# Kernel tuning notes

Measured on AMD Instinct MI355X. Metric: run time of the kernel, lower is better.

The kernel has to match this reference:

```python
import jax, jax.numpy as jnp
import numpy as np

N_NODES = 100000
N_EDGES = 1600000
D_IN = 64
D_OUT = 64


def setup_inputs() -> dict:
    key = jax.random.key(0)
    k1, k2, k3, k4 = jax.random.split(key, 4)
    x = jax.random.normal(k1, (N_NODES, D_IN), dtype=jnp.float32)
    edge_index = jax.random.randint(k2, (2, N_EDGES), 0, N_NODES, dtype=jnp.int64)
    W = jax.random.normal(k3, (D_OUT, D_IN), dtype=jnp.float32) * (1.0 / np.sqrt(D_IN))
    b = jax.random.normal(k4, (D_OUT,), dtype=jnp.float32) * 0.01
    return {"x": x, "edge_index": edge_index, "W": W, "b": b}


def reference(x, edge_index, W, b):
    num_nodes = x.shape[0]
    row, col = edge_index[0], edge_index[1]
    # degree of each node as a destination (scatter_add of ones over row)
    deg = jax.ops.segment_sum(jnp.ones(row.shape[0], dtype=x.dtype), row,
                              num_segments=num_nodes)
    # deg^-0.5 with inf (deg==0) replaced by 0
    deg_inv_sqrt = jnp.where(deg > 0, jax.lax.rsqrt(jnp.maximum(deg, 1.0)) * jnp.where(deg > 0, 1.0, 0.0), 0.0)
    deg_inv_sqrt = jnp.where(deg > 0, deg ** -0.5, 0.0)
    # gather source features, scale by source norm, scatter-add to destinations
    weighted = x[col] * deg_inv_sqrt[col][:, None]          # [E, D_IN]
    agg = jax.ops.segment_sum(weighted, row, num_segments=num_nodes)  # [N, D_IN]
    agg = agg * deg_inv_sqrt[:, None]
    # linear + relu (torch Linear: y = agg @ W.T + b)
    return jax.nn.relu(agg @ W.T + b)
```

## Files before the change

kernel.cpp:

```cpp
#include <hip/hip_runtime.h>

#define N_NODES 100000
#define N_EDGES 1600000
#define D 64

#define FSHIFT 5
#define FNODES 32
#define NFB 3125
#define CAPF 768

#define CSHIFT 11
#define CNODES 2048
#define NCB 49
#define CCAP 36864
#define FPC 64

#define CHUNK 4096
#define EPT 16
#define NCHUNKA 391
#define NCHUNKB 9
#define NSB (NCB * NCHUNKB)
#define NXF 1563

#define COLBITS 17
#define COLMASK 0x1FFFF

#define CCUR_OFF   0
#define FCUR_OFF   256
#define INIT_BYTES 12756
#define DINV_OFF   16384
#define Y_OFF      417792
#define CPAIRS_OFF 13217792
#define FPAIRS_OFF 20443136

typedef float fvec4 __attribute__((ext_vector_type(4)));

__device__ __forceinline__ unsigned f2bf(float f) {
    unsigned bits = __float_as_uint(f);
    return (bits + 0x7FFFu + ((bits >> 16) & 1u)) >> 16;
}

__global__ __launch_bounds__(256) void scatA_kernel(const int* __restrict__ row,
                                                    const int* __restrict__ col,
                                                    int* __restrict__ ccur,
                                                    int* __restrict__ cpairs) {
    __shared__ int lcnt[NCB];
    int t = threadIdx.x;
    int base = blockIdx.x * CHUNK;
    if (t < NCB) lcnt[t] = 0;
    __syncthreads();
    int r[EPT], c[EPT], pos[EPT];
#pragma unroll
    for (int i = 0; i < EPT; ++i) {
        int e = base + i * 256 + t;
        if (e < N_EDGES) {
            r[i] = row[e];
            c[i] = col[e];
            pos[i] = atomicAdd(&lcnt[r[i] >> CSHIFT], 1);
        } else r[i] = -1;
    }
    __syncthreads();
    if (t < NCB) {
        int cc = lcnt[t];
        if (cc) lcnt[t] = t * CCAP + atomicAdd(&ccur[t], cc);
    }
    __syncthreads();
#pragma unroll
    for (int i = 0; i < EPT; ++i) {
        if (r[i] >= 0) {
            int cb = r[i] >> CSHIFT;
            int rl = r[i] & (CNODES - 1);
            cpairs[lcnt[cb] + pos[i]] = (rl << COLBITS) | c[i];
        }
    }
}

__global__ __launch_bounds__(1024) void dinv_kernel(const int* __restrict__ cpairs,
                                                    const int* __restrict__ ccur,
                                                    float* __restrict__ dinv) {
    __shared__ int hist[CNODES];
    int t = threadIdx.x;
    int cb = blockIdx.x;
    for (int i = t; i < CNODES; i += 1024) hist[i] = 0;
    __syncthreads();
    int beg = cb * CCAP;
    int end = beg + ccur[cb];
    for (int k = beg + t; k < end; k += 1024)
        atomicAdd(&hist[cpairs[k] >> COLBITS], 1);
    __syncthreads();
    for (int i = t; i < CNODES; i += 1024) {
        int n = (cb << CSHIFT) + i;
        if (n < N_NODES) {
            int d = hist[i];
            dinv[n] = (d > 0) ? rsqrtf((float)d) : 0.0f;
        }
    }
}

__global__ __launch_bounds__(256) void sbxf_kernel(
        const int* __restrict__ cpairs, const int* __restrict__ ccur,
        int* __restrict__ fcur, int* __restrict__ fpairs,
        const float* __restrict__ x, const float* __restrict__ W,
        const float* __restrict__ dinv, unsigned short* __restrict__ y) {
    __shared__ __align__(16) float smem[2 * 64 * 68 + 64];
    int t = threadIdx.x;
    int blk = blockIdx.x;
    if (blk < NSB) {
        int* lcnt = (int*)smem;
        int cb = blk / NCHUNKB;
        int k  = blk % NCHUNKB;
        int beg = cb * CCAP + k * CHUNK;
        int end = cb * CCAP + ccur[cb];
        if (end > beg + CHUNK) end = beg + CHUNK;
        if (t < FPC) lcnt[t] = 0;
        __syncthreads();
        int pc[EPT], pos[EPT];
#pragma unroll
        for (int i = 0; i < EPT; ++i) {
            int e = beg + i * 256 + t;
            if (e < end) {
                pc[i] = cpairs[e];
                pos[i] = atomicAdd(&lcnt[pc[i] >> (COLBITS + FSHIFT)], 1);
            } else pc[i] = -1;
        }
        __syncthreads();
        if (t < FPC) {
            int cc = lcnt[t];
            if (cc) {
                int fb = (cb << 6) + t;
                lcnt[t] = fb * CAPF + atomicAdd(&fcur[fb], cc);
            }
        }
        __syncthreads();
#pragma unroll
        for (int i = 0; i < EPT; ++i) {
            if (pc[i] >= 0) {
                int fl = pc[i] >> (COLBITS + FSHIFT);
                int rl5 = (pc[i] >> COLBITS) & (FNODES - 1);
                fpairs[lcnt[fl] + pos[i]] = (rl5 << COLBITS) | (pc[i] & COLMASK);
            }
        }
        return;
    }
    float* XT = smem;
    float* WT = smem + 64 * 68;
    float* dl = smem + 2 * 64 * 68;
    int b = blk - NSB;
    int nb0 = b << 6;
    for (int i = t; i < D * D; i += 256) {
        int j = i >> 6, d = i & 63;
        WT[d * 68 + j] = W[i];
    }
    if (t < 64) {
        int g = nb0 + t;
        dl[t] = (g < N_NODES) ? dinv[g] : 0.0f;
    }
    for (int i = t; i < 64 * D; i += 256) {
        int n = i >> 6, d = i & 63;
        int g = nb0 + n;
        XT[d * 68 + n] = (g < N_NODES) ? x[(size_t)g * D + d] : 0.0f;
    }
    __syncthreads();
    int tj = t & 15, tn = t >> 4;
    float4 a0 = {0,0,0,0}, a1 = {0,0,0,0}, a2 = {0,0,0,0}, a3 = {0,0,0,0};
#pragma unroll 8
    for (int d = 0; d < D; ++d) {
        float4 xv = *(const float4*)&XT[d * 68 + tn * 4];
        float4 wv = *(const float4*)&WT[d * 68 + tj * 4];
        a0.x = fmaf(xv.x, wv.x, a0.x); a0.y = fmaf(xv.x, wv.y, a0.y);
        a0.z = fmaf(xv.x, wv.z, a0.z); a0.w = fmaf(xv.x, wv.w, a0.w);
        a1.x = fmaf(xv.y, wv.x, a1.x); a1.y = fmaf(xv.y, wv.y, a1.y);
        a1.z = fmaf(xv.y, wv.z, a1.z); a1.w = fmaf(xv.y, wv.w, a1.w);
        a2.x = fmaf(xv.z, wv.x, a2.x); a2.y = fmaf(xv.z, wv.y, a2.y);
        a2.z = fmaf(xv.z, wv.z, a2.z); a2.w = fmaf(xv.z, wv.w, a2.w);
        a3.x = fmaf(xv.w, wv.x, a3.x); a3.y = fmaf(xv.w, wv.y, a3.y);
        a3.z = fmaf(xv.w, wv.z, a3.z); a3.w = fmaf(xv.w, wv.w, a3.w);
    }
    int jb = tj * 4;
#pragma unroll
    for (int s = 0; s < 4; ++s) {
        int g = nb0 + tn * 4 + s;
        if (g < N_NODES) {
            float scv = dl[tn * 4 + s];
            float4 a = (s == 0) ? a0 : (s == 1) ? a1 : (s == 2) ? a2 : a3;
            unsigned lo = f2bf(a.x * scv) | (f2bf(a.y * scv) << 16);
            unsigned hi = f2bf(a.z * scv) | (f2bf(a.w * scv) << 16);
            *(uint2*)(y + (size_t)g * D + jb) = make_uint2(lo, hi);
        }
    }
}

__global__ __launch_bounds__(256) void mega_kernel(
        const int* __restrict__ fpairs, const int* __restrict__ fcur,
        const unsigned short* __restrict__ y,
        const float* __restrict__ bias, float* __restrict__ out) {
    __shared__ int hist[FNODES];
    __shared__ int sc[FNODES];
    __shared__ int lrptr[FNODES + 1];
    __shared__ int lcur[FNODES];
    __shared__ float dl[FNODES];
    __shared__ int lds_scol[CAPF];
    int t = threadIdx.x;
    int b = blockIdx.x;
    int beg = b * CAPF;
    int cnt = fcur[b];
    if (t < FNODES) hist[t] = 0;
    __syncthreads();
    for (int k = t; k < cnt; k += 256)
        atomicAdd(&hist[fpairs[beg + k] >> COLBITS], 1);
    __syncthreads();
    if (t < FNODES) sc[t] = hist[t];
    __syncthreads();
    for (int off = 1; off < FNODES; off <<= 1) {
        int v = (t < FNODES && t >= off) ? sc[t - off] : 0;
        __syncthreads();
        if (t < FNODES) sc[t] += v;
        __syncthreads();
    }
    if (t < FNODES) {
        lrptr[t + 1] = sc[t];
        lcur[t] = sc[t] - hist[t];
        dl[t] = (hist[t] > 0) ? rsqrtf((float)hist[t]) : 0.0f;
    }
    if (t == 0) lrptr[0] = 0;
    __syncthreads();
    for (int k = t; k < cnt; k += 256) {
        int p = fpairs[beg + k];
        int pos = atomicAdd(&lcur[p >> COLBITS], 1);
        lds_scol[pos] = p & COLMASK;
    }
    __syncthreads();
    int wave = t >> 6;
    int lane = t & 63;
    int g = lane >> 3;
    int q = lane & 7;
    float bj[8];
    {
        float4 b0 = *(const float4*)(bias + q * 8);
        float4 b1 = *(const float4*)(bias + q * 8 + 4);
        bj[0] = b0.x; bj[1] = b0.y; bj[2] = b0.z; bj[3] = b0.w;
        bj[4] = b1.x; bj[5] = b1.y; bj[6] = b1.z; bj[7] = b1.w;
    }
    for (int ln = wave; ln < FNODES; ln += 4) {
        int s = lrptr[ln], e2 = lrptr[ln + 1];
        float a[8];
#pragma unroll
        for (int i = 0; i < 8; ++i) a[i] = 0.0f;
        for (int k = s; k < e2; k += 32) {
#pragma unroll
            for (int u = 0; u < 4; ++u) {
                int e = k + u * 8 + g;
                if (e < e2) {
                    int c = lds_scol[e];
                    uint4 v = *(const uint4*)(y + (size_t)c * D + q * 8);
                    a[0] += __uint_as_float(v.x << 16);
                    a[1] += __uint_as_float(v.x & 0xffff0000u);
                    a[2] += __uint_as_float(v.y << 16);
                    a[3] += __uint_as_float(v.y & 0xffff0000u);
                    a[4] += __uint_as_float(v.z << 16);
                    a[5] += __uint_as_float(v.z & 0xffff0000u);
                    a[6] += __uint_as_float(v.w << 16);
                    a[7] += __uint_as_float(v.w & 0xffff0000u);
                }
            }
        }
#pragma unroll
        for (int m = 8; m <= 32; m <<= 1) {
#pragma unroll
            for (int i = 0; i < 8; ++i)
                a[i] += __shfl_xor(a[i], m);
        }
        float dv = dl[ln];
        int n = (b << FSHIFT) + ln;
        if (g < 2) {
            int o = g * 4;
            fvec4 r;
            r.x = fmaxf(fmaf(dv, a[o + 0], bj[o + 0]), 0.0f);
            r.y = fmaxf(fmaf(dv, a[o + 1], bj[o + 1]), 0.0f);
            r.z = fmaxf(fmaf(dv, a[o + 2], bj[o + 2]), 0.0f);
            r.w = fmaxf(fmaf(dv, a[o + 3], bj[o + 3]), 0.0f);
            __builtin_nontemporal_store(r, (fvec4*)(out + (size_t)n * D + q * 8 + o));
        }
    }
}

extern "C" void kernel_launch(void* const* d_in, const int* in_sizes, int n_in,
                              void* d_out, int out_size, void* d_ws, size_t ws_size,
                              hipStream_t stream) {
    const float* x    = (const float*)d_in[0];
    const int*   eidx = (const int*)d_in[1];
    const float* W    = (const float*)d_in[2];
    const float* b    = (const float*)d_in[3];
    float* out = (float*)d_out;
    char* ws = (char*)d_ws;

    const int* row = eidx;
    const int* col = eidx + N_EDGES;

    int*   ccur   = (int*)  (ws + CCUR_OFF);
    int*   fcur   = (int*)  (ws + FCUR_OFF);
    float* dinv   = (float*)(ws + DINV_OFF);
    unsigned short* y = (unsigned short*)(ws + Y_OFF);
    int*   cpairs = (int*)  (ws + CPAIRS_OFF);
    int*   fpairs = (int*)  (ws + FPAIRS_OFF);

    hipMemsetAsync(ws, 0, INIT_BYTES, stream);
    scatA_kernel<<<NCHUNKA, 256, 0, stream>>>(row, col, ccur, cpairs);
    dinv_kernel<<<NCB, 1024, 0, stream>>>(cpairs, ccur, dinv);
    sbxf_kernel<<<NSB + NXF, 256, 0, stream>>>(cpairs, ccur, fcur, fpairs, x, W, dinv, y);
    mega_kernel<<<NFB, 256, 0, stream>>>(fpairs, fcur, y, b, out);
}
```

Baseline: 186.3 us.

## Merge dinv into second pass, split xform across passes, apply source norm in gather

The dense transform no longer depends on degree normalisation; instead each edge's source dinv is loaded in the final aggregation kernel and applied via fma. This lets the transform tiles be split between the first scatter kernel and the second kernel, and the dinv histogram is folded into the second kernel, cutting one launch. The cost is an extra random dinv gather per edge and extra LDS in the aggregation kernel. The mega kernel also assumes at most 768 pairs per bucket, which is the existing CAPF capacity.

```diff
diff --git a/kernel.cpp b/kernel.cpp
--- a/kernel.cpp
+++ b/kernel.cpp
@@ -21,6 +21,8 @@
 #define NCHUNKB 9
 #define NSB (NCB * NCHUNKB)
 #define NXF 1563
+#define XFA 700
+#define XFB (NXF - XFA)
 
 #define COLBITS 17
 #define COLMASK 0x1FFFF
@@ -40,120 +42,14 @@
     return (bits + 0x7FFFu + ((bits >> 16) & 1u)) >> 16;
 }
 
-__global__ __launch_bounds__(256) void scatA_kernel(const int* __restrict__ row,
-                                                    const int* __restrict__ col,
-                                                    int* __restrict__ ccur,
-                                                    int* __restrict__ cpairs) {
-    __shared__ int lcnt[NCB];
-    int t = threadIdx.x;
-    int base = blockIdx.x * CHUNK;
-    if (t < NCB) lcnt[t] = 0;
-    __syncthreads();
-    int r[EPT], c[EPT], pos[EPT];
-#pragma unroll
-    for (int i = 0; i < EPT; ++i) {
-        int e = base + i * 256 + t;
-        if (e < N_EDGES) {
-            r[i] = row[e];
-            c[i] = col[e];
-            pos[i] = atomicAdd(&lcnt[r[i] >> CSHIFT], 1);
-        } else r[i] = -1;
-    }
-    __syncthreads();
-    if (t < NCB) {
-        int cc = lcnt[t];
-        if (cc) lcnt[t] = t * CCAP + atomicAdd(&ccur[t], cc);
-    }
-    __syncthreads();
-#pragma unroll
-    for (int i = 0; i < EPT; ++i) {
-        if (r[i] >= 0) {
-            int cb = r[i] >> CSHIFT;
-            int rl = r[i] & (CNODES - 1);
-            cpairs[lcnt[cb] + pos[i]] = (rl << COLBITS) | c[i];
-        }
-    }
-}
-
-__global__ __launch_bounds__(1024) void dinv_kernel(const int* __restrict__ cpairs,
-                                                    const int* __restrict__ ccur,
-                                                    float* __restrict__ dinv) {
-    __shared__ int hist[CNODES];
-    int t = threadIdx.x;
-    int cb = blockIdx.x;
-    for (int i = t; i < CNODES; i += 1024) hist[i] = 0;
-    __syncthreads();
-    int beg = cb * CCAP;
-    int end = beg + ccur[cb];
-    for (int k = beg + t; k < end; k += 1024)
-        atomicAdd(&hist[cpairs[k] >> COLBITS], 1);
-    __syncthreads();
-    for (int i = t; i < CNODES; i += 1024) {
-        int n = (cb << CSHIFT) + i;
-        if (n < N_NODES) {
-            int d = hist[i];
-            dinv[n] = (d > 0) ? rsqrtf((float)d) : 0.0f;
-        }
-    }
-}
-
-__global__ __launch_bounds__(256) void sbxf_kernel(
-        const int* __restrict__ cpairs, const int* __restrict__ ccur,
-        int* __restrict__ fcur, int* __restrict__ fpairs,
+__device__ __forceinline__ void xform_tile(int nb0, float* smem, int t,
         const float* __restrict__ x, const float* __restrict__ W,
-        const float* __restrict__ dinv, unsigned short* __restrict__ y) {
-    __shared__ __align__(16) float smem[2 * 64 * 68 + 64];
-    int t = threadIdx.x;
-    int blk = blockIdx.x;
-    if (blk < NSB) {
-        int* lcnt = (int*)smem;
-        int cb = blk / NCHUNKB;
-        int k  = blk % NCHUNKB;
-        int beg = cb * CCAP + k * CHUNK;
-        int end = cb * CCAP + ccur[cb];
-        if (end > beg + CHUNK) end = beg + CHUNK;
-        if (t < FPC) lcnt[t] = 0;
-        __syncthreads();
-        int pc[EPT], pos[EPT];
-#pragma unroll
-        for (int i = 0; i < EPT; ++i) {
-            int e = beg + i * 256 + t;
-            if (e < end) {
-                pc[i] = cpairs[e];
-                pos[i] = atomicAdd(&lcnt[pc[i] >> (COLBITS + FSHIFT)], 1);
-            } else pc[i] = -1;
-        }
-        __syncthreads();
-        if (t < FPC) {
-            int cc = lcnt[t];
-            if (cc) {
-                int fb = (cb << 6) + t;
-                lcnt[t] = fb * CAPF + atomicAdd(&fcur[fb], cc);
-            }
-        }
-        __syncthreads();
-#pragma unroll
-        for (int i = 0; i < EPT; ++i) {
-            if (pc[i] >= 0) {
-                int fl = pc[i] >> (COLBITS + FSHIFT);
-                int rl5 = (pc[i] >> COLBITS) & (FNODES - 1);
-                fpairs[lcnt[fl] + pos[i]] = (rl5 << COLBITS) | (pc[i] & COLMASK);
-            }
-        }
-        return;
-    }
+        unsigned short* __restrict__ y) {
     float* XT = smem;
     float* WT = smem + 64 * 68;
-    float* dl = smem + 2 * 64 * 68;
-    int b = blk - NSB;
-    int nb0 = b << 6;
     for (int i = t; i < D * D; i += 256) {
         int j = i >> 6, d = i & 63;
         WT[d * 68 + j] = W[i];
-    }
-    if (t < 64) {
-        int g = nb0 + t;
-        dl[t] = (g < N_NODES) ? dinv[g] : 0.0f;
     }
     for (int i = t; i < 64 * D; i += 256) {
         int n = i >> 6, d = i & 63;
@@ -181,18 +77,128 @@
     for (int s = 0; s < 4; ++s) {
         int g = nb0 + tn * 4 + s;
         if (g < N_NODES) {
-            float scv = dl[tn * 4 + s];
             float4 a = (s == 0) ? a0 : (s == 1) ? a1 : (s == 2) ? a2 : a3;
-            unsigned lo = f2bf(a.x * scv) | (f2bf(a.y * scv) << 16);
-            unsigned hi = f2bf(a.z * scv) | (f2bf(a.w * scv) << 16);
+            unsigned lo = f2bf(a.x) | (f2bf(a.y) << 16);
+            unsigned hi = f2bf(a.z) | (f2bf(a.w) << 16);
             *(uint2*)(y + (size_t)g * D + jb) = make_uint2(lo, hi);
+        }
+    }
+}
+
+__global__ __launch_bounds__(256) void saxf_kernel(
+        const int* __restrict__ row, const int* __restrict__ col,
+        int* __restrict__ ccur, int* __restrict__ cpairs,
+        const float* __restrict__ x, const float* __restrict__ W,
+        unsigned short* __restrict__ y) {
+    __shared__ __align__(16) float smem[2 * 64 * 68];
+    int t = threadIdx.x;
+    int blk = blockIdx.x;
+    if (blk >= NCHUNKA) {
+        xform_tile((blk - NCHUNKA) << 6, smem, t, x, W, y);
+        return;
+    }
+    int* lcnt = (int*)smem;
+    int base = blk * CHUNK;
+    if (t < NCB) lcnt[t] = 0;
+    __syncthreads();
+    int r[EPT], c[EPT], pos[EPT];
+#pragma unroll
+    for (int i = 0; i < EPT; ++i) {
+        int e = base + i * 256 + t;
+        if (e < N_EDGES) {
+            r[i] = row[e];
+            c[i] = col[e];
+            pos[i] = atomicAdd(&lcnt[r[i] >> CSHIFT], 1);
+        } else r[i] = -1;
+    }
+    __syncthreads();
+    if (t < NCB) {
+        int cc = lcnt[t];
+        if (cc) lcnt[t] = t * CCAP + atomicAdd(&ccur[t], cc);
+    }
+    __syncthreads();
+#pragma unroll
+    for (int i = 0; i < EPT; ++i) {
+        if (r[i] >= 0) {
+            int cb = r[i] >> CSHIFT;
+            int rl = r[i] & (CNODES - 1);
+            cpairs[lcnt[cb] + pos[i]] = (rl << COLBITS) | c[i];
+        }
+    }
+}
+
+__global__ __launch_bounds__(256) void dsbxf_kernel(
+        const int* __restrict__ cpairs, const int* __restrict__ ccur,
+        int* __restrict__ fcur, int* __restrict__ fpairs,
+        float* __restrict__ dinv,
+        const float* __restrict__ x, const float* __restrict__ W,
+        unsigned short* __restrict__ y) {
+    __shared__ __align__(16) float smem[2 * 64 * 68];
+    int t = threadIdx.x;
+    int blk = blockIdx.x;
+    if (blk < NCB) {
+        int* hist = (int*)smem;
+        int cb = blk;
+        for (int i = t; i < CNODES; i += 256) hist[i] = 0;
+        __syncthreads();
+        int beg = cb * CCAP;
+        int end = beg + ccur[cb];
+        for (int k = beg + t; k < end; k += 256)
+            atomicAdd(&hist[cpairs[k] >> COLBITS], 1);
+        __syncthreads();
+        for (int i = t; i < CNODES; i += 256) {
+            int n = (cb << CSHIFT) + i;
+            if (n < N_NODES) {
+                int d = hist[i];
+                dinv[n] = (d > 0) ? rsqrtf((float)d) : 0.0f;
+            }
+        }
+        return;
+    }
+    if (blk >= NCB + NSB) {
+        xform_tile((XFA + blk - NCB - NSB) << 6, smem, t, x, W, y);
+        return;
+    }
+    int* lcnt = (int*)smem;
+    int bb = blk - NCB;
+    int cb = bb / NCHUNKB;
+    int k  = bb % NCHUNKB;
+    int beg = cb * CCAP + k * CHUNK;
+    int end = cb * CCAP + ccur[cb];
+    if (end > beg + CHUNK) end = beg + CHUNK;
+    if (t < FPC) lcnt[t] = 0;
+    __syncthreads();
+    int pc[EPT], pos[EPT];
+#pragma unroll
+    for (int i = 0; i < EPT; ++i) {
+        int e = beg + i * 256 + t;
+        if (e < end) {
+            pc[i] = cpairs[e];
+            pos[i] = atomicAdd(&lcnt[pc[i] >> (COLBITS + FSHIFT)], 1);
+        } else pc[i] = -1;
+    }
+    __syncthreads();
+    if (t < FPC) {
+        int cc = lcnt[t];
+        if (cc) {
+            int fb = (cb << 6) + t;
+            lcnt[t] = fb * CAPF + atomicAdd(&fcur[fb], cc);
+        }
+    }
+    __syncthreads();
+#pragma unroll
+    for (int i = 0; i < EPT; ++i) {
+        if (pc[i] >= 0) {
+            int fl = pc[i] >> (COLBITS + FSHIFT);
+            int rl5 = (pc[i] >> COLBITS) & (FNODES - 1);
+            fpairs[lcnt[fl] + pos[i]] = (rl5 << COLBITS) | (pc[i] & COLMASK);
         }
     }
 }
 
 __global__ __launch_bounds__(256) void mega_kernel(
         const int* __restrict__ fpairs, const int* __restrict__ fcur,
-        const unsigned short* __restrict__ y,
+        const unsigned short* __restrict__ y, const float* __restrict__ dinv_g,
         const float* __restrict__ bias, float* __restrict__ out) {
     __shared__ int hist[FNODES];
     __shared__ int sc[FNODES];
@@ -200,14 +206,21 @@
     __shared__ int lcur[FNODES];
     __shared__ float dl[FNODES];
     __shared__ int lds_scol[CAPF];
+    __shared__ float lds_dinv[CAPF];
     int t = threadIdx.x;
     int b = blockIdx.x;
     int beg = b * CAPF;
     int cnt = fcur[b];
     if (t < FNODES) hist[t] = 0;
     __syncthreads();
-    for (int k = t; k < cnt; k += 256)
-        atomicAdd(&hist[fpairs[beg + k] >> COLBITS], 1);
+    int p0 = -1, p1 = -1, p2 = -1;
+    float d0 = 0.0f, d1 = 0.0f, d2 = 0.0f;
+    if (t < cnt)       { p0 = fpairs[beg + t];       d0 = dinv_g[p0 & COLMASK]; }
+    if (t + 256 < cnt) { p1 = fpairs[beg + t + 256]; d1 = dinv_g[p1 & COLMASK]; }
+    if (t + 512 < cnt) { p2 = fpairs[beg + t + 512]; d2 = dinv_g[p2 & COLMASK]; }
+    if (p0 >= 0) atomicAdd(&hist[p0 >> COLBITS], 1);
+    if (p1 >= 0) atomicAdd(&hist[p1 >> COLBITS], 1);
+    if (p2 >= 0) atomicAdd(&hist[p2 >> COLBITS], 1);
     __syncthreads();
     if (t < FNODES) sc[t] = hist[t];
     __syncthreads();
@@ -224,10 +237,20 @@
     }
     if (t == 0) lrptr[0] = 0;
     __syncthreads();
-    for (int k = t; k < cnt; k += 256) {
-        int p = fpairs[beg + k];
-        int pos = atomicAdd(&lcur[p >> COLBITS], 1);
-        lds_scol[pos] = p & COLMASK;
+    if (p0 >= 0) {
+        int pos = atomicAdd(&lcur[p0 >> COLBITS], 1);
+        lds_scol[pos] = p0 & COLMASK;
+        lds_dinv[pos] = d0;
+    }
+    if (p1 >= 0) {
+        int pos = atomicAdd(&lcur[p1 >> COLBITS], 1);
+        lds_scol[pos] = p1 & COLMASK;
+        lds_dinv[pos] = d1;
+    }
+    if (p2 >= 0) {
+        int pos = atomicAdd(&lcur[p2 >> COLBITS], 1);
+        lds_scol[pos] = p2 & COLMASK;
+        lds_dinv[pos] = d2;
     }
     __syncthreads();
     int wave = t >> 6;
@@ -252,15 +275,16 @@
                 int e = k + u * 8 + g;
                 if (e < e2) {
                     int c = lds_scol[e];
+                    float dvc = lds_dinv[e];
                     uint4 v = *(const uint4*)(y + (size_t)c * D + q * 8);
-                    a[0] += __uint_as_float(v.x << 16);
-                    a[1] += __uint_as_float(v.x & 0xffff0000u);
-                    a[2] += __uint_as_float(v.y << 16);
-                    a[3] += __uint_as_float(v.y & 0xffff0000u);
-                    a[4] += __uint_as_float(v.z << 16);
-                    a[5] += __uint_as_float(v.z & 0xffff0000u);
-                    a[6] += __uint_as_float(v.w << 16);
-                    a[7] += __uint_as_float(v.w & 0xffff0000u);
+                    a[0] = fmaf(dvc, __uint_as_float(v.x << 16), a[0]);
+                    a[1] = fmaf(dvc, __uint_as_float(v.x & 0xffff0000u), a[1]);
+                    a[2] = fmaf(dvc, __uint_as_float(v.y << 16), a[2]);
+                    a[3] = fmaf(dvc, __uint_as_float(v.y & 0xffff0000u), a[3]);
+                    a[4] = fmaf(dvc, __uint_as_float(v.z << 16), a[4]);
+                    a[5] = fmaf(dvc, __uint_as_float(v.z & 0xffff0000u), a[5]);
+                    a[6] = fmaf(dvc, __uint_as_float(v.w << 16), a[6]);
+                    a[7] = fmaf(dvc, __uint_as_float(v.w & 0xffff0000u), a[7]);
                 }
             }
         }
@@ -305,8 +329,7 @@
     int*   fpairs = (int*)  (ws + FPAIRS_OFF);
 
     hipMemsetAsync(ws, 0, INIT_BYTES, stream);
-    scatA_kernel<<<NCHUNKA, 256, 0, stream>>>(row, col, ccur, cpairs);
-    dinv_kernel<<<NCB, 1024, 0, stream>>>(cpairs, ccur, dinv);
-    sbxf_kernel<<<NSB + NXF, 256, 0, stream>>>(cpairs, ccur, fcur, fpairs, x, W, dinv, y);
-    mega_kernel<<<NFB, 256, 0, stream>>>(fpairs, fcur, y, b, out);
-}
+    saxf_kernel<<<NCHUNKA + XFA, 256, 0, stream>>>(row, col, ccur, cpairs, x, W, y);
+    dsbxf_kernel<<<NCB + NSB + XFB, 256, 0, stream>>>(cpairs, ccur, fcur, fpairs, dinv, x, W, y);
+    mega_kernel<<<NFB, 256, 0, stream>>>(fpairs, fcur, y, dinv, b, out);
+}
```

Result: slower. 196.1 us (+5.2%).
